# Kernel optimization log

Hardware: AMD Instinct MI355X
Metric: run time of the kernel (lower is better)

Reference implementation:

```python
import jax, jax.numpy as jnp
import numpy as np

B, N = 4, 2048
PARAM_G = 0.125       # recovery rate
VIRUS_DEATH = 8e-5    # disease-induced death rate


def setup_inputs() -> dict:
    key = jax.random.key(0)
    ks = jax.random.split(key, 7)
    return {
        "param_b": jax.random.uniform(ks[0], (B, N, 1), jnp.float32),
        "contact": jax.random.uniform(ks[1], (B, N, 1), jnp.float32),
        "mob": jax.random.uniform(ks[2], (B, N, N), jnp.float32),
        "SIR": jax.random.uniform(ks[3], (B, N, 4), jnp.float32),
        "sps": jax.random.uniform(ks[4], (B, N, N), jnp.float32),
        # original loads birth_china.npy / death_china.npy and divides by 365000
        "nature_birth": jax.random.uniform(ks[5], (N, 1), jnp.float32) / 365000.0,
        "nature_death": jax.random.uniform(ks[6], (N, 1), jnp.float32) / 365000.0,
    }


def reference(param_b, contact, mob, SIR, sps, nature_birth, nature_death):
    b, n = SIR.shape[0], SIR.shape[1]
    eye = jnp.eye(n, dtype=bool)
    # zero out diagonal (no self-mobility)
    F_nm = jnp.where(eye[None], 0.0, mob)            # [B,N,N]
    sps_m = jnp.where(eye[None], 0.0, sps)           # [B,N,N]
    # torch: P = F_nm / F_nm.sum(1).unsqueeze(2)  -> divide row i,col j by sum_k F[b,k,j] broadcast over last dim
    col_sum = F_nm.sum(axis=1)                       # [B,N]
    P = F_nm / col_sum[:, :, None]                   # [B,N,N]
    fai = F_nm.sum(axis=(1, 2))[:, None]             # [B,1]

    S = SIR[..., 0:1]
    I = SIR[..., 1:2]
    R = SIR[..., 2:3]
    I_sum = SIR[..., 3:4]
    pop = S + I + R                                  # [B,N,1]
    tau = pop.sum(axis=1)                            # [B,1]
    m = (fai / tau)[:, :, None]                      # [B,1,1] mobility rate (scalar per batch)

    birth = nature_birth[None]                       # [1,N,1]
    death = nature_death[None]                       # [1,N,1]

    I_new = S / pop * param_b * contact * I          # new infections

    # flux term: sum_j m * X[b,j] * P[b,i,j] == m * (P @ X), fused matvec instead of [B,N,N] broadcast
    flux = lambda X: m * jnp.matmul(P, X)            # [B,N,1]

    R_t = R + PARAM_G * I - death * R - m * R + flux(R)
    I_t = I + I_new - death * I - PARAM_G * I - VIRUS_DEATH * I - m * I + flux(I)
    S_t = S - I_new - death * S + birth * pop - m * S + flux(S)
    I_sum_t = I_sum + I_new

    R0 = param_b * contact / (death + PARAM_G + VIRUS_DEATH + m)
    W_arrive = param_b * contact - death - PARAM_G - VIRUS_DEATH

    Ht_SIR = jnp.concatenate([R0, I_new, S_t, I_t, R_t, I_sum_t], axis=-1)       # [B,N,6]
    arrive1 = jnp.concatenate(
        [W_arrive, jnp.broadcast_to(m, S.shape), I, pop], axis=-1)               # [B,N,4]
    arrive2 = jnp.stack([sps_m, P], axis=-1)                                     # [B,N,N,2]
    return Ht_SIR, arrive1, arrive2
```

## Files before the change

### kernel.cpp

```cpp
#include <hip/hip_runtime.h>

#define NN 2048
#define BB 4
#define PARAM_G 0.125f
#define VIRUS_DEATH 8e-5f

#define WS_ROWS 8192
#define WS_ROWI 16384
#define WS_ROWR 24576
#define WS_FAI  32768
#define WS_TAU  32772
#define WS_ZERO_FLOATS (WS_TAU + BB)

__global__ __launch_bounds__(256) void k_colsum(const float* __restrict__ mob,
                                                float* ws) {
    int t  = threadIdx.x;
    int i0 = blockIdx.x * 32;
    int j  = blockIdx.y * 1024 + t * 4;
    int b  = blockIdx.z;
    const float* base = mob + ((size_t)b * NN + i0) * NN + j;
    float4 acc = make_float4(0.f, 0.f, 0.f, 0.f);
    #pragma unroll 8
    for (int r = 0; r < 32; ++r) {
        float4 v = *(const float4*)(base + (size_t)r * NN);
        unsigned d = (unsigned)((i0 + r) - j);
        if (d < 4u) ((float*)&v)[d] = 0.0f;
        acc.x += v.x; acc.y += v.y; acc.z += v.z; acc.w += v.w;
    }
    atomicAdd(&ws[b * NN + j + 0], acc.x);
    atomicAdd(&ws[b * NN + j + 1], acc.y);
    atomicAdd(&ws[b * NN + j + 2], acc.z);
    atomicAdd(&ws[b * NN + j + 3], acc.w);
    float s = acc.x + acc.y + acc.z + acc.w;
    for (int off = 32; off; off >>= 1) s += __shfl_down(s, off);
    if ((t & 63) == 0) atomicAdd(&ws[WS_FAI + b], s);
}

__global__ __launch_bounds__(256) void k_tau(const float* __restrict__ SIR,
                                             float* ws) {
    int b  = blockIdx.x >> 2;
    int n0 = (blockIdx.x & 3) * 512;
    int t  = threadIdx.x;
    float acc = 0.f;
    #pragma unroll
    for (int k = 0; k < 2; ++k) {
        int n = n0 + k * 256 + t;
        float4 s = *(const float4*)(SIR + ((size_t)b * NN + n) * 4);
        acc += s.x + s.y + s.z;
    }
    for (int off = 32; off; off >>= 1) acc += __shfl_down(acc, off);
    __shared__ float red[4];
    int w = t >> 6;
    if ((t & 63) == 0) red[w] = acc;
    __syncthreads();
    if (t == 0) atomicAdd(&ws[WS_TAU + b], red[0] + red[1] + red[2] + red[3]);
}

__global__ __launch_bounds__(256) void k_main(const float* __restrict__ mob,
                                              const float* __restrict__ sps,
                                              const float* __restrict__ SIR,
                                              float* ws,
                                              float* __restrict__ out2) {
    __shared__ __align__(16) float sS[NN];
    __shared__ __align__(16) float sI[NN];
    __shared__ __align__(16) float sR[NN];
    int t = threadIdx.x;
    int b = blockIdx.y;
    for (int j = t; j < NN; j += 256) {
        float4 s = *(const float4*)(SIR + ((size_t)b * NN + j) * 4);
        sS[j] = s.x; sI[j] = s.y; sR[j] = s.z;
    }
    __syncthreads();

    int w = t >> 6, lane = t & 63;
    int i0 = blockIdx.x * 8;
    #pragma unroll
    for (int k = 0; k < 2; ++k) {
        int i = i0 + w + 4 * k;
        float invc = 1.0f / ws[b * NN + i];
        size_t rowoff = ((size_t)b * NN + i) * NN;
        const float* mrow = mob + rowoff;
        const float* srow = sps + rowoff;
        float* orow = out2 + rowoff * 2;
        float aS = 0.f, aI = 0.f, aR = 0.f;
        #pragma unroll 4
        for (int iter = 0; iter < 16; ++iter) {
            int j2 = iter * 128 + lane * 2;
            float2 mv = *(const float2*)(mrow + j2);
            float2 sv = *(const float2*)(srow + j2);
            unsigned d = (unsigned)(i - j2);
            if (d == 0u)      { mv.x = 0.f; sv.x = 0.f; }
            else if (d == 1u) { mv.y = 0.f; sv.y = 0.f; }
            float2 xS = *(const float2*)&sS[j2];
            float2 xI = *(const float2*)&sI[j2];
            float2 xR = *(const float2*)&sR[j2];
            aS += mv.x * xS.x + mv.y * xS.y;
            aI += mv.x * xI.x + mv.y * xI.y;
            aR += mv.x * xR.x + mv.y * xR.y;
            *(float4*)(orow + (size_t)j2 * 2) =
                make_float4(sv.x, mv.x * invc, sv.y, mv.y * invc);
        }
        for (int off = 32; off; off >>= 1) {
            aS += __shfl_down(aS, off);
            aI += __shfl_down(aI, off);
            aR += __shfl_down(aR, off);
        }
        if (lane == 0) {
            ws[WS_ROWS + b * NN + i] = aS;
            ws[WS_ROWI + b * NN + i] = aI;
            ws[WS_ROWR + b * NN + i] = aR;
        }
    }
}

__global__ __launch_bounds__(256) void k_epi(const float* __restrict__ param_b,
                                             const float* __restrict__ contact,
                                             const float* __restrict__ SIR,
                                             const float* __restrict__ nb,
                                             const float* __restrict__ nd,
                                             const float* ws,
                                             float* __restrict__ out0,
                                             float* __restrict__ out1) {
    int g = blockIdx.x * 256 + threadIdx.x;
    int b = g >> 11;
    int n = g & (NN - 1);
    float4 sir = *(const float4*)(SIR + (size_t)g * 4);
    float S = sir.x, I = sir.y, R = sir.z, Isum = sir.w;
    float pb = param_b[g], ct = contact[g];
    float birth = nb[n], death = nd[n];
    float cs = ws[g];
    float rS = ws[WS_ROWS + g], rI = ws[WS_ROWI + g], rR = ws[WS_ROWR + g];
    float m = ws[WS_FAI + b] / ws[WS_TAU + b];

    float pop   = S + I + R;
    float pbc   = pb * ct;
    float I_new = S / pop * pbc * I;
    float icv   = 1.0f / cs;
    float fS = m * rS * icv, fI = m * rI * icv, fR = m * rR * icv;

    float R_t    = R + PARAM_G * I - death * R - m * R + fR;
    float I_t    = I + I_new - death * I - PARAM_G * I - VIRUS_DEATH * I - m * I + fI;
    float S_t    = S - I_new - death * S + birth * pop - m * S + fS;
    float Isum_t = Isum + I_new;
    float R0     = pbc / (death + PARAM_G + VIRUS_DEATH + m);
    float W      = pbc - death - PARAM_G - VIRUS_DEATH;

    float* o0 = out0 + (size_t)g * 6;
    *(float2*)(o0 + 0) = make_float2(R0, I_new);
    *(float2*)(o0 + 2) = make_float2(S_t, I_t);
    *(float2*)(o0 + 4) = make_float2(R_t, Isum_t);
    *(float4*)(out1 + (size_t)g * 4) = make_float4(W, m, I, pop);
}

extern "C" void kernel_launch(void* const* d_in, const int* in_sizes, int n_in,
                              void* d_out, int out_size, void* d_ws, size_t ws_size,
                              hipStream_t stream) {
    const float* param_b = (const float*)d_in[0];
    const float* contact = (const float*)d_in[1];
    const float* mob     = (const float*)d_in[2];
    const float* SIR     = (const float*)d_in[3];
    const float* sps     = (const float*)d_in[4];
    const float* nb      = (const float*)d_in[5];
    const float* nd      = (const float*)d_in[6];

    float* out  = (float*)d_out;
    float* out0 = out;
    float* out1 = out + (size_t)BB * NN * 6;
    float* out2 = out1 + (size_t)BB * NN * 4;
    float* ws   = (float*)d_ws;

    hipMemsetAsync(ws, 0, (size_t)WS_ZERO_FLOATS * sizeof(float), stream);

    k_colsum<<<dim3(64, 2, BB),  256, 0, stream>>>(mob, ws);
    k_tau   <<<16,               256, 0, stream>>>(SIR, ws);
    k_main  <<<dim3(NN / 8, BB), 256, 0, stream>>>(mob, sps, SIR, ws, out2);
    k_epi   <<<(BB * NN) / 256,  256, 0, stream>>>(param_b, contact, SIR, nb, nd,
                                                   ws, out0, out1);
}
```

Measured before the change: 295.1 us.

## Fuse tau into colsum and epilogue into main kernel, add nontemporal streams

Folds the tau reduction into the column-sum kernel (one block per batch computes it) and moves the per-node epidemic epilogue into the main matvec kernel, so lane 0 writes the outputs directly. This drops two kernel launches and the workspace round trip for row sums. The column-sum grid is doubled with half the rows per block for more parallelism. The sps load and the out2 store now use nontemporal hints to reduce cache pollution from the large streamed arrays.

```diff
diff --git a/kernel.cpp b/kernel.cpp
--- a/kernel.cpp
+++ b/kernel.cpp
@@ -5,23 +5,24 @@
 #define PARAM_G 0.125f
 #define VIRUS_DEATH 8e-5f
 
-#define WS_ROWS 8192
-#define WS_ROWI 16384
-#define WS_ROWR 24576
-#define WS_FAI  32768
-#define WS_TAU  32772
-#define WS_ZERO_FLOATS (WS_TAU + BB)
+typedef float nfloat2 __attribute__((ext_vector_type(2)));
+typedef float nfloat4 __attribute__((ext_vector_type(4)));
+
+#define WS_FAI  8192
+#define WS_TAU  8196
+#define WS_ZERO_FLOATS 8200
 
 __global__ __launch_bounds__(256) void k_colsum(const float* __restrict__ mob,
+                                                const float* __restrict__ SIR,
                                                 float* ws) {
     int t  = threadIdx.x;
-    int i0 = blockIdx.x * 32;
+    int i0 = blockIdx.x * 16;
     int j  = blockIdx.y * 1024 + t * 4;
     int b  = blockIdx.z;
     const float* base = mob + ((size_t)b * NN + i0) * NN + j;
     float4 acc = make_float4(0.f, 0.f, 0.f, 0.f);
-    #pragma unroll 8
-    for (int r = 0; r < 32; ++r) {
+    #pragma unroll
+    for (int r = 0; r < 16; ++r) {
         float4 v = *(const float4*)(base + (size_t)r * NN);
         unsigned d = (unsigned)((i0 + r) - j);
         if (d < 4u) ((float*)&v)[d] = 0.0f;
@@ -34,32 +35,32 @@
     float s = acc.x + acc.y + acc.z + acc.w;
     for (int off = 32; off; off >>= 1) s += __shfl_down(s, off);
     if ((t & 63) == 0) atomicAdd(&ws[WS_FAI + b], s);
-}
-
-__global__ __launch_bounds__(256) void k_tau(const float* __restrict__ SIR,
-                                             float* ws) {
-    int b  = blockIdx.x >> 2;
-    int n0 = (blockIdx.x & 3) * 512;
-    int t  = threadIdx.x;
-    float acc = 0.f;
-    #pragma unroll
-    for (int k = 0; k < 2; ++k) {
-        int n = n0 + k * 256 + t;
-        float4 s = *(const float4*)(SIR + ((size_t)b * NN + n) * 4);
-        acc += s.x + s.y + s.z;
+    if (blockIdx.x == 0 && blockIdx.y == 0) {
+        float accT = 0.f;
+        #pragma unroll
+        for (int k = 0; k < 8; ++k) {
+            int n = k * 256 + t;
+            float4 sv = *(const float4*)(SIR + ((size_t)b * NN + n) * 4);
+            accT += sv.x + sv.y + sv.z;
+        }
+        for (int off = 32; off; off >>= 1) accT += __shfl_down(accT, off);
+        __shared__ float red[4];
+        if ((t & 63) == 0) red[t >> 6] = accT;
+        __syncthreads();
+        if (t == 0) ws[WS_TAU + b] = red[0] + red[1] + red[2] + red[3];
     }
-    for (int off = 32; off; off >>= 1) acc += __shfl_down(acc, off);
-    __shared__ float red[4];
-    int w = t >> 6;
-    if ((t & 63) == 0) red[w] = acc;
-    __syncthreads();
-    if (t == 0) atomicAdd(&ws[WS_TAU + b], red[0] + red[1] + red[2] + red[3]);
 }
 
 __global__ __launch_bounds__(256) void k_main(const float* __restrict__ mob,
                                               const float* __restrict__ sps,
                                               const float* __restrict__ SIR,
-                                              float* ws,
+                                              const float* __restrict__ param_b,
+                                              const float* __restrict__ contact,
+                                              const float* __restrict__ nb,
+                                              const float* __restrict__ nd,
+                                              const float* ws,
+                                              float* __restrict__ out0,
+                                              float* __restrict__ out1,
                                               float* __restrict__ out2) {
     __shared__ __align__(16) float sS[NN];
     __shared__ __align__(16) float sI[NN];
@@ -74,6 +75,7 @@
 
     int w = t >> 6, lane = t & 63;
     int i0 = blockIdx.x * 8;
+    float m = ws[WS_FAI + b] / ws[WS_TAU + b];
     #pragma unroll
     for (int k = 0; k < 2; ++k) {
         int i = i0 + w + 4 * k;
@@ -87,7 +89,7 @@
         for (int iter = 0; iter < 16; ++iter) {
             int j2 = iter * 128 + lane * 2;
             float2 mv = *(const float2*)(mrow + j2);
-            float2 sv = *(const float2*)(srow + j2);
+            nfloat2 sv = __builtin_nontemporal_load((const nfloat2*)(srow + j2));
             unsigned d = (unsigned)(i - j2);
             if (d == 0u)      { mv.x = 0.f; sv.x = 0.f; }
             else if (d == 1u) { mv.y = 0.f; sv.y = 0.f; }
@@ -97,8 +99,8 @@
             aS += mv.x * xS.x + mv.y * xS.y;
             aI += mv.x * xI.x + mv.y * xI.y;
             aR += mv.x * xR.x + mv.y * xR.y;
-            *(float4*)(orow + (size_t)j2 * 2) =
-                make_float4(sv.x, mv.x * invc, sv.y, mv.y * invc);
+            nfloat4 o = { sv.x, mv.x * invc, sv.y, mv.y * invc };
+            __builtin_nontemporal_store(o, (nfloat4*)(orow + (size_t)j2 * 2));
         }
         for (int off = 32; off; off >>= 1) {
             aS += __shfl_down(aS, off);
@@ -106,50 +108,29 @@
             aR += __shfl_down(aR, off);
         }
         if (lane == 0) {
-            ws[WS_ROWS + b * NN + i] = aS;
-            ws[WS_ROWI + b * NN + i] = aI;
-            ws[WS_ROWR + b * NN + i] = aR;
+            int g = b * NN + i;
+            float4 sir = *(const float4*)(SIR + (size_t)g * 4);
+            float S = sir.x, I = sir.y, R = sir.z, Isum = sir.w;
+            float pb = param_b[g], ct = contact[g];
+            float birth = nb[i], death = nd[i];
+            float pop   = S + I + R;
+            float pbc   = pb * ct;
+            float I_new = S / pop * pbc * I;
+            float fS = m * aS * invc, fI = m * aI * invc, fR = m * aR * invc;
+            float R_t    = R + PARAM_G * I - death * R - m * R + fR;
+            float I_t    = I + I_new - death * I - PARAM_G * I - VIRUS_DEATH * I
+                             - m * I + fI;
+            float S_t    = S - I_new - death * S + birth * pop - m * S + fS;
+            float Isum_t = Isum + I_new;
+            float R0     = pbc / (death + PARAM_G + VIRUS_DEATH + m);
+            float W      = pbc - death - PARAM_G - VIRUS_DEATH;
+            float* o0 = out0 + (size_t)g * 6;
+            *(float2*)(o0 + 0) = make_float2(R0, I_new);
+            *(float2*)(o0 + 2) = make_float2(S_t, I_t);
+            *(float2*)(o0 + 4) = make_float2(R_t, Isum_t);
+            *(float4*)(out1 + (size_t)g * 4) = make_float4(W, m, I, pop);
         }
     }
-}
-
-__global__ __launch_bounds__(256) void k_epi(const float* __restrict__ param_b,
-                                             const float* __restrict__ contact,
-                                             const float* __restrict__ SIR,
-                                             const float* __restrict__ nb,
-                                             const float* __restrict__ nd,
-                                             const float* ws,
-                                             float* __restrict__ out0,
-                                             float* __restrict__ out1) {
-    int g = blockIdx.x * 256 + threadIdx.x;
-    int b = g >> 11;
-    int n = g & (NN - 1);
-    float4 sir = *(const float4*)(SIR + (size_t)g * 4);
-    float S = sir.x, I = sir.y, R = sir.z, Isum = sir.w;
-    float pb = param_b[g], ct = contact[g];
-    float birth = nb[n], death = nd[n];
-    float cs = ws[g];
-    float rS = ws[WS_ROWS + g], rI = ws[WS_ROWI + g], rR = ws[WS_ROWR + g];
-    float m = ws[WS_FAI + b] / ws[WS_TAU + b];
-
-    float pop   = S + I + R;
-    float pbc   = pb * ct;
-    float I_new = S / pop * pbc * I;
-    float icv   = 1.0f / cs;
-    float fS = m * rS * icv, fI = m * rI * icv, fR = m * rR * icv;
-
-    float R_t    = R + PARAM_G * I - death * R - m * R + fR;
-    float I_t    = I + I_new - death * I - PARAM_G * I - VIRUS_DEATH * I - m * I + fI;
-    float S_t    = S - I_new - death * S + birth * pop - m * S + fS;
-    float Isum_t = Isum + I_new;
-    float R0     = pbc / (death + PARAM_G + VIRUS_DEATH + m);
-    float W      = pbc - death - PARAM_G - VIRUS_DEATH;
-
-    float* o0 = out0 + (size_t)g * 6;
-    *(float2*)(o0 + 0) = make_float2(R0, I_new);
-    *(float2*)(o0 + 2) = make_float2(S_t, I_t);
-    *(float2*)(o0 + 4) = make_float2(R_t, Isum_t);
-    *(float4*)(out1 + (size_t)g * 4) = make_float4(W, m, I, pop);
 }
 
 extern "C" void kernel_launch(void* const* d_in, const int* in_sizes, int n_in,
@@ -169,11 +150,9 @@
     float* out2 = out1 + (size_t)BB * NN * 4;
     float* ws   = (float*)d_ws;
 
-    hipMemsetAsync(ws, 0, (size_t)WS_ZERO_FLOATS * sizeof(float), stream);
+    (void)hipMemsetAsync(ws, 0, (size_t)WS_ZERO_FLOATS * sizeof(float), stream);
 
-    k_colsum<<<dim3(64, 2, BB),  256, 0, stream>>>(mob, ws);
-    k_tau   <<<16,               256, 0, stream>>>(SIR, ws);
-    k_main  <<<dim3(NN / 8, BB), 256, 0, stream>>>(mob, sps, SIR, ws, out2);
-    k_epi   <<<(BB * NN) / 256,  256, 0, stream>>>(param_b, contact, SIR, nb, nd,
-                                                   ws, out0, out1);
+    k_colsum<<<dim3(128, 2, BB), 256, 0, stream>>>(mob, SIR, ws);
+    k_main  <<<dim3(NN / 8, BB), 256, 0, stream>>>(mob, sps, SIR, param_b, contact,
+                                                   nb, nd, ws, out0, out1, out2);
 }
```

Measured after the change: 306.3 us. +3.8%, slower.
